# Performance work log

Hardware: AMD Instinct MI355X
Metric: run time of the kernel (lower is better)

The kernel has to match this reference:

```python
import jax, jax.numpy as jnp
import numpy as np

C, B, D = 1_000_000, 4096, 128

def setup_inputs() -> dict:
    key = jax.random.key(0)
    ks = jax.random.split(key, 7)
    nodes = jax.random.normal(ks[0], (C, D), dtype=jnp.float32)
    z_local = jax.random.normal(ks[1], (B, D), dtype=jnp.float32)
    z_meta = jax.random.normal(ks[2], (D,), dtype=jnp.float32)
    # MLP params: Linear(3D -> D), GELU, Linear(D -> 1)
    W1 = jax.random.normal(ks[3], (3 * D, D), dtype=jnp.float32) / np.sqrt(3 * D)
    b1 = jnp.zeros((D,), dtype=jnp.float32)
    W2 = jax.random.normal(ks[4], (D, 1), dtype=jnp.float32) / np.sqrt(D)
    b2 = jnp.zeros((1,), dtype=jnp.float32)
    batch = jnp.sort(jax.random.randint(ks[5], (C,), 0, B, dtype=jnp.int64))
    return {"nodes": nodes, "z_local": z_local, "z_meta": z_meta,
            "W1": W1, "b1": b1, "W2": W2, "b2": b2, "batch": batch}

def reference(nodes, z_local, z_meta, W1, b1, W2, b2, batch):
    # gather per-graph global vector for each node, broadcast batch-wide meta
    z_local_tiled = z_local[batch]                       # [C, D]
    z_meta_tiled = jnp.broadcast_to(z_meta[None, :], nodes.shape)  # [C, D]
    combined = jnp.concatenate([nodes, z_local_tiled, z_meta_tiled], axis=-1)  # [C, 3D]
    h = jax.nn.gelu(combined @ W1 + b1, approximate=False)  # [C, D]
    logits = (h @ W2 + b2).squeeze(-1)                       # [C]
    return logits
```

## Files before the change

kernel.cpp:

```cpp
#include <hip/hip_runtime.h>
#include <hip/hip_bf16.h>
#include <cstdint>


typedef __attribute__((ext_vector_type(8))) __bf16 bf16x8;
typedef __attribute__((ext_vector_type(4))) float f32x4;
typedef __attribute__((address_space(3))) uint32_t lds_u32;
typedef __attribute__((address_space(1))) const uint32_t glob_u32;

#define D_DIM 128

__device__ __forceinline__ float gelu_exact(float x) {
    float t = 0.70710678118654752f * x;
    float a = fabsf(t);
    float d = __builtin_amdgcn_rcpf(fmaf(0.3275911f, a, 1.0f));
    float p = fmaf(1.061405429f, d, -1.453152027f);
    p = fmaf(p, d, 1.421413741f);
    p = fmaf(p, d, -0.284496736f);
    p = fmaf(p, d, 0.254829592f);
    p = p * d;
    float e = __builtin_amdgcn_exp2f(a * a * -1.4426950408889634f);
    float erf_a = fmaf(-p, e, 1.0f);
    float erf_t = copysignf(erf_a, t);
    return 0.5f * x * (1.0f + erf_t);
}

__global__ __launch_bounds__(256) void prep_all(
    const float* __restrict__ z_local, const float* __restrict__ z_meta,
    const float* __restrict__ W1, const float* __restrict__ b1,
    __bf16* __restrict__ w1f, float* __restrict__ bias2, float* __restrict__ pre) {
    const int blk = blockIdx.x;
    const int tid = threadIdx.x;
    if (blk < 64) {
        int f = blk * 256 + tid;
        int j = f & 7, lane = (f >> 3) & 63, nt = (f >> 9) & 7, kc = f >> 12;
        int k = kc * 32 + (lane >> 4) * 8 + j;
        int n = nt * 16 + (lane & 15);
        w1f[f] = (__bf16)W1[k * D_DIM + n];
    } else if (blk == 64) {
        if (tid < D_DIM) {
            int n = tid;
            float s = b1[n];
            for (int k = 0; k < D_DIM; ++k)
                s = fmaf(z_meta[k], W1[(2 * D_DIM + k) * D_DIM + n], s);
            bias2[n] = s;
        }
    } else {
        int pb = blk - 65;
        int n = tid & 127;
        int g0 = pb * 8 + (tid >> 7) * 4;
        float s[4] = {0.f, 0.f, 0.f, 0.f};
        for (int k = 0; k < D_DIM; ++k) {
            float wk = W1[(D_DIM + k) * D_DIM + n];
#pragma unroll
            for (int g = 0; g < 4; ++g)
                s[g] = fmaf(z_local[(size_t)(g0 + g) * D_DIM + k], wk, s[g]);
        }
#pragma unroll
        for (int g = 0; g < 4; ++g) pre[(size_t)(g0 + g) * D_DIM + n] = s[g];
    }
}

__global__ __launch_bounds__(256) void readout_main(
    const float* __restrict__ nodes, const int* __restrict__ batch,
    const float* __restrict__ pre, const __bf16* __restrict__ w1f,
    const float* __restrict__ bias2, const float* __restrict__ W2,
    const float* __restrict__ b2, float* __restrict__ out) {
    __shared__ __bf16 w1s[16384];
    const int tid = threadIdx.x;
    const int wave = tid >> 6;
    const int lane = tid & 63;
    const int q = lane >> 4;
    const int c0 = lane & 15;
    const int row_base = blockIdx.x * 64 + wave * 16;

    const float* aptr = nodes + (size_t)(row_base + c0) * D_DIM + q * 8;
    f32x4 a[8];
#pragma unroll
    for (int kc = 0; kc < 4; ++kc) {
        a[2 * kc]     = *((const f32x4*)(aptr + kc * 32));
        a[2 * kc + 1] = *((const f32x4*)(aptr + kc * 32 + 4));
    }

    {
        const __bf16* gsrc = w1f + wave * 4096;
        __bf16* ldst = w1s + wave * 4096;
#pragma unroll
        for (int it = 0; it < 8; ++it) {
            __builtin_amdgcn_global_load_lds(
                (glob_u32*)(gsrc + it * 512 + lane * 8),
                (lds_u32*)(ldst + it * 512), 16, 0, 0);
        }
    }

    int brow[4];
#pragma unroll
    for (int r = 0; r < 4; ++r) brow[r] = batch[row_base + q * 4 + r];
    float w2v[8], bz[8];
#pragma unroll
    for (int nt = 0; nt < 8; ++nt) {
        w2v[nt] = W2[nt * 16 + c0];
        bz[nt]  = bias2[nt * 16 + c0];
    }
    const float b2v = b2[0];

    __syncthreads();

    f32x4 acc[8] = {};
    const bf16x8* bfr = (const bf16x8*)w1s;
#pragma unroll
    for (int kc = 0; kc < 4; ++kc) {
        bf16x8 af;
#pragma unroll
        for (int j = 0; j < 8; ++j)
            af[j] = (__bf16)a[2 * kc + (j >> 2)][j & 3];
#pragma unroll
        for (int nt = 0; nt < 8; ++nt) {
            bf16x8 bf = bfr[(kc * 8 + nt) * 64 + lane];
            acc[nt] = __builtin_amdgcn_mfma_f32_16x16x32_bf16(af, bf, acc[nt], 0, 0, 0);
        }
    }

#pragma unroll
    for (int r = 0; r < 4; ++r) {
        const float* prow = pre + (size_t)brow[r] * D_DIM;
        float partial = 0.f;
#pragma unroll
        for (int nt = 0; nt < 8; ++nt) {
            float u = acc[nt][r] + prow[nt * 16 + c0] + bz[nt];
            partial += gelu_exact(u) * w2v[nt];
        }
        partial += __shfl_xor(partial, 1);
        partial += __shfl_xor(partial, 2);
        partial += __shfl_xor(partial, 4);
        partial += __shfl_xor(partial, 8);
        if (c0 == 0) out[row_base + q * 4 + r] = partial + b2v;
    }
}

extern "C" void kernel_launch(void* const* d_in, const int* in_sizes, int n_in,
                              void* d_out, int out_size, void* d_ws, size_t ws_size,
                              hipStream_t stream) {
    const float* nodes   = (const float*)d_in[0];
    const float* z_local = (const float*)d_in[1];
    const float* z_meta  = (const float*)d_in[2];
    const float* W1      = (const float*)d_in[3];
    const float* b1      = (const float*)d_in[4];
    const float* W2      = (const float*)d_in[5];
    const float* b2      = (const float*)d_in[6];
    const int*   batch   = (const int*)d_in[7];
    float* out = (float*)d_out;

    char* ws = (char*)d_ws;
    __bf16* w1f  = (__bf16*)ws;
    float* bias2 = (float*)(ws + 32768);
    float* pre   = (float*)(ws + 33280);

    prep_all<<<577, 256, 0, stream>>>(z_local, z_meta, W1, b1, w1f, bias2, pre);
    readout_main<<<15625, 256, 0, stream>>>(nodes, batch, pre, w1f, bias2, W2, b2, out);
}
```

Before: 690.7 us.

## Make readout kernel persistent with double-buffered register prefetch of node tiles

Replaces the one-tile-per-wave grid of 15625 blocks with a persistent grid of 1792 blocks. Each wave loops over 16-row tiles, loading the next tile's node rows and batch indices into registers while the current tile runs through MFMA and GELU. W1 is staged into LDS once per block instead of once per 64 rows, which cuts redundant weight traffic and launch overhead. The cost is higher register pressure from the two register buffers, which may lower occupancy, and a fixed grid size that may not match the number of CUs.

```diff
diff --git a/kernel.cpp b/kernel.cpp
--- a/kernel.cpp
+++ b/kernel.cpp
@@ -9,6 +9,7 @@
 typedef __attribute__((address_space(1))) const uint32_t glob_u32;
 
 #define D_DIM 128
+#define NT_TILES 62500
 
 __device__ __forceinline__ float gelu_exact(float x) {
     float t = 0.70710678118654752f * x;
@@ -61,51 +62,27 @@
     }
 }
 
-__global__ __launch_bounds__(256) void readout_main(
-    const float* __restrict__ nodes, const int* __restrict__ batch,
-    const float* __restrict__ pre, const __bf16* __restrict__ w1f,
-    const float* __restrict__ bias2, const float* __restrict__ W2,
-    const float* __restrict__ b2, float* __restrict__ out) {
-    __shared__ __bf16 w1s[16384];
-    const int tid = threadIdx.x;
-    const int wave = tid >> 6;
-    const int lane = tid & 63;
-    const int q = lane >> 4;
-    const int c0 = lane & 15;
-    const int row_base = blockIdx.x * 64 + wave * 16;
-
-    const float* aptr = nodes + (size_t)(row_base + c0) * D_DIM + q * 8;
-    f32x4 a[8];
+__device__ __forceinline__ void load_tile(const float* __restrict__ nodes,
+                                          const int* __restrict__ batch,
+                                          int t, int q, int c0,
+                                          f32x4 a[8], int brow[4]) {
+    const float* aptr = nodes + (size_t)(t * 16 + c0) * D_DIM + q * 8;
 #pragma unroll
     for (int kc = 0; kc < 4; ++kc) {
         a[2 * kc]     = *((const f32x4*)(aptr + kc * 32));
         a[2 * kc + 1] = *((const f32x4*)(aptr + kc * 32 + 4));
     }
+#pragma unroll
+    for (int r = 0; r < 4; ++r) brow[r] = batch[t * 16 + q * 4 + r];
+}
 
-    {
-        const __bf16* gsrc = w1f + wave * 4096;
-        __bf16* ldst = w1s + wave * 4096;
-#pragma unroll
-        for (int it = 0; it < 8; ++it) {
-            __builtin_amdgcn_global_load_lds(
-                (glob_u32*)(gsrc + it * 512 + lane * 8),
-                (lds_u32*)(ldst + it * 512), 16, 0, 0);
-        }
-    }
-
-    int brow[4];
-#pragma unroll
-    for (int r = 0; r < 4; ++r) brow[r] = batch[row_base + q * 4 + r];
-    float w2v[8], bz[8];
-#pragma unroll
-    for (int nt = 0; nt < 8; ++nt) {
-        w2v[nt] = W2[nt * 16 + c0];
-        bz[nt]  = bias2[nt * 16 + c0];
-    }
-    const float b2v = b2[0];
-
-    __syncthreads();
-
+__device__ __forceinline__ void compute_tile(const __bf16* w1s,
+                                             const float* __restrict__ pre,
+                                             float* __restrict__ out,
+                                             int t, int lane, int q, int c0,
+                                             const f32x4 a[8], const int brow[4],
+                                             const float w2v[8], const float bz[8],
+                                             float b2v) {
     f32x4 acc[8] = {};
     const bf16x8* bfr = (const bf16x8*)w1s;
 #pragma unroll
@@ -120,7 +97,6 @@
             acc[nt] = __builtin_amdgcn_mfma_f32_16x16x32_bf16(af, bf, acc[nt], 0, 0, 0);
         }
     }
-
 #pragma unroll
     for (int r = 0; r < 4; ++r) {
         const float* prow = pre + (size_t)brow[r] * D_DIM;
@@ -134,7 +110,61 @@
         partial += __shfl_xor(partial, 2);
         partial += __shfl_xor(partial, 4);
         partial += __shfl_xor(partial, 8);
-        if (c0 == 0) out[row_base + q * 4 + r] = partial + b2v;
+        if (c0 == 0) out[t * 16 + q * 4 + r] = partial + b2v;
+    }
+}
+
+__global__ __launch_bounds__(256) void readout_main(
+    const float* __restrict__ nodes, const int* __restrict__ batch,
+    const float* __restrict__ pre, const __bf16* __restrict__ w1f,
+    const float* __restrict__ bias2, const float* __restrict__ W2,
+    const float* __restrict__ b2, float* __restrict__ out) {
+    __shared__ __bf16 w1s[16384];
+    const int tid = threadIdx.x;
+    const int wave = tid >> 6;
+    const int lane = tid & 63;
+    const int q = lane >> 4;
+    const int c0 = lane & 15;
+
+    {
+        const __bf16* gsrc = w1f + wave * 4096;
+        __bf16* ldst = w1s + wave * 4096;
+#pragma unroll
+        for (int it = 0; it < 8; ++it) {
+            __builtin_amdgcn_global_load_lds(
+                (glob_u32*)(gsrc + it * 512 + lane * 8),
+                (lds_u32*)(ldst + it * 512), 16, 0, 0);
+        }
+    }
+    float w2v[8], bz[8];
+#pragma unroll
+    for (int nt = 0; nt < 8; ++nt) {
+        w2v[nt] = W2[nt * 16 + c0];
+        bz[nt]  = bias2[nt * 16 + c0];
+    }
+    const float b2v = b2[0];
+    __syncthreads();
+
+    const int NW = gridDim.x * 4;
+    int t = blockIdx.x * 4 + wave;
+    if (t >= NT_TILES) return;
+
+    f32x4 a0[8], a1[8];
+    int br0[4], br1[4];
+    load_tile(nodes, batch, t, q, c0, a0, br0);
+
+    while (true) {
+        int t2 = t + NW;
+        if (t2 < NT_TILES) load_tile(nodes, batch, t2, q, c0, a1, br1);
+        compute_tile(w1s, pre, out, t, lane, q, c0, a0, br0, w2v, bz, b2v);
+        t = t2;
+        if (t >= NT_TILES) break;
+
+        t2 = t + NW;
+        if (t2 < NT_TILES) load_tile(nodes, batch, t2, q, c0, a0, br0);
+        compute_tile(w1s, pre, out, t, lane, q, c0, a1, br1, w2v, bz, b2v);
+        t = t2;
+        if (t >= NT_TILES) break;
     }
 }
 
@@ -157,5 +187,5 @@
     float* pre   = (float*)(ws + 33280);
 
     prep_all<<<577, 256, 0, stream>>>(z_local, z_meta, W1, b1, w1f, bias2, pre);
-    readout_main<<<15625, 256, 0, stream>>>(nodes, batch, pre, w1f, bias2, W2, b2, out);
+    readout_main<<<1792, 256, 0, stream>>>(nodes, batch, pre, w1f, bias2, W2, b2, out);
 }
```

After: 936.3 us. 35.6% more time.
